# Optimization experiments

Measured on AMD Instinct MI355X. Metric: run time of the kernel, lower is better.

Reference implementation:

```python
import jax, jax.numpy as jnp
import numpy as np

SEQ, EMB, QKV = 4096, 1024, 1024

def setup_inputs() -> dict:
    key = jax.random.key(0)
    k_x, k_q, k_k, k_v = jax.random.split(key, 4)
    scale = 1.0 / np.sqrt(EMB)
    return {
        "x": jax.random.normal(k_x, (SEQ, EMB), dtype=jnp.float32),
        "W_q": jax.random.normal(k_q, (EMB, QKV), dtype=jnp.float32) * scale,
        "W_k": jax.random.normal(k_k, (EMB, QKV), dtype=jnp.float32) * scale,
        "W_v": jax.random.normal(k_v, (EMB, QKV), dtype=jnp.float32) * scale,
    }

def reference(x, W_q, W_k, W_v):
    # Single-head scaled dot-product attention, unbatched: x [S, E]
    d_k = W_q.shape[1]
    Q = x @ W_q          # [S, D]
    K = x @ W_k          # [S, D]
    V = x @ W_v          # [S, D]
    scores = (Q @ K.T) * (1.0 / jnp.sqrt(jnp.asarray(d_k, dtype=x.dtype)))  # [S, S]
    attn = jax.nn.softmax(scores, axis=-1)
    return attn @ V      # [S, D]
```

## Files before the change

### kernel.cpp

```cpp
#include <hip/hip_runtime.h>
#include <cstdint>

#define S_DIM 4096
#define E_DIM 1024
#define D_DIM 1024

typedef __bf16 bf16x8 __attribute__((ext_vector_type(8)));
typedef float  f32x4  __attribute__((ext_vector_type(4)));
typedef unsigned short u16x8 __attribute__((ext_vector_type(8)));

__device__ __forceinline__ unsigned short f2bf(float f) {
  unsigned u = __float_as_uint(f);
  unsigned r = (u + 0x7fffu + ((u >> 16) & 1u)) >> 16;
  return (unsigned short)r;
}

__device__ __forceinline__ void lds_copy16(const unsigned short* g, const unsigned short* l) {
  auto gp = reinterpret_cast<__attribute__((address_space(1))) unsigned int*>(
      reinterpret_cast<uintptr_t>(g));
  auto lp = reinterpret_cast<__attribute__((address_space(3))) unsigned int*>(
      reinterpret_cast<uintptr_t>(l));
  __builtin_amdgcn_global_load_lds(gp, lp, 16, 0, 0);
}

__global__ __launch_bounds__(256) void prep_kernel(
    const float* __restrict__ x,
    const float* __restrict__ Wq, const float* __restrict__ Wk, const float* __restrict__ Wv,
    unsigned short* __restrict__ xbf, unsigned short* __restrict__ Wt,
    float* __restrict__ lsum) {
  const int z = blockIdx.z;
  const int tid = threadIdx.x;
  if (z < 3) {
    const float* W = (z == 0) ? Wq : (z == 1 ? Wk : Wv);
    unsigned short* out = Wt + (size_t)z * E_DIM * D_DIM;
    __shared__ unsigned short tile[32][33];
    int bc = blockIdx.x * 32, br = blockIdx.y * 32;
    int tx = tid & 31, ty = tid >> 5;
#pragma unroll
    for (int i = 0; i < 32; i += 8)
      tile[ty + i][tx] = f2bf(W[(size_t)(br + ty + i) * D_DIM + bc + tx]);
    __syncthreads();
#pragma unroll
    for (int i = 0; i < 32; i += 8)
      out[(size_t)(bc + ty + i) * E_DIM + br + tx] = tile[tx][ty + i];
  } else {
    int bid = blockIdx.y * 32 + blockIdx.x;
    int i = (bid * 256 + tid) * 16;
#pragma unroll
    for (int h = 0; h < 2; h++) {
      float4 a = *(const float4*)(x + i + h * 8);
      float4 b = *(const float4*)(x + i + h * 8 + 4);
      u16x8 o;
      o[0] = f2bf(a.x); o[1] = f2bf(a.y); o[2] = f2bf(a.z); o[3] = f2bf(a.w);
      o[4] = f2bf(b.x); o[5] = f2bf(b.y); o[6] = f2bf(b.z); o[7] = f2bf(b.w);
      *(u16x8*)(xbf + i + h * 8) = o;
    }
    if (bid < 16) lsum[bid * 256 + tid] = 0.f;
  }
}

__global__ __launch_bounds__(256) void transpose_bf16_kernel(
    const unsigned short* __restrict__ in, unsigned short* __restrict__ out,
    int ldin, int ldout) {
  __shared__ unsigned short tile[32][33];
  int bc = blockIdx.x * 32, br = blockIdx.y * 32;
  int tx = threadIdx.x & 31, ty = threadIdx.x >> 5;
#pragma unroll
  for (int i = 0; i < 32; i += 8)
    tile[ty + i][tx] = in[(size_t)(br + ty + i) * ldin + bc + tx];
  __syncthreads();
#pragma unroll
  for (int i = 0; i < 32; i += 8)
    out[(size_t)(bc + ty + i) * ldout + br + tx] = tile[tx][ty + i];
}

template <int MODE, bool SPLIT3>
__global__ __launch_bounds__(256, 2) void gemm_bt_kernel(
    const unsigned short* __restrict__ A, int lda,
    const unsigned short* __restrict__ Bt, int ldb,
    void* __restrict__ Cp, unsigned short* __restrict__ C1,
    unsigned short* __restrict__ C2, int ldc,
    int Kper, float scale, float* __restrict__ lsum) {
  __shared__ __align__(16) unsigned short sA[128 * 64];
  __shared__ __align__(16) unsigned short sB[128 * 64];

  const int tid = threadIdx.x;

  int flat = blockIdx.y * gridDim.x + blockIdx.x;
  int numInG = 8 * gridDim.x;
  int g = flat / numInG;
  int r = flat - g * numInG;
  const int bm = (g * 8 + (r & 7)) * 128;
  const int bn = (r >> 3) * 128;

  const int wave = tid >> 6;
  const int lane = tid & 63;
  const int q    = lane >> 4;
  const int l16  = lane & 15;
  const int wm   = (wave >> 1) * 64;
  const int wn   = (wave & 1) * 64;

  f32x4 zero = {0.f, 0.f, 0.f, 0.f};
  f32x4 acc[4][4];
#pragma unroll
  for (int t = 0; t < 4; t++)
#pragma unroll
    for (int u = 0; u < 4; u++) acc[t][u] = zero;

  const int srow   = tid >> 3;
  const int schunk = (tid & 7) ^ (srow & 3);
  const int kbase  = blockIdx.z * Kper;
  const unsigned short* ap = A  + (size_t)(bm + srow) * lda + kbase + schunk * 8;
  const unsigned short* bp = Bt + (size_t)(bn + srow) * ldb + kbase + schunk * 8;
  unsigned short* saw = sA + wave * 512;
  unsigned short* sbw = sB + wave * 512;
  const size_t stepA = (size_t)32 * lda;
  const size_t stepB = (size_t)32 * ldb;

  const int sw = (q ^ (l16 & 3)) * 8;

  for (int k0 = 0; k0 < Kper; k0 += 64) {
#pragma unroll
    for (int p = 0; p < 4; p++) {
      lds_copy16(ap + k0 + p * stepA, saw + p * 2048);
      lds_copy16(bp + k0 + p * stepB, sbw + p * 2048);
    }
    __syncthreads();

#pragma unroll
    for (int h = 0; h < 2; h++) {
      bf16x8 af[4], bfv[4];
#pragma unroll
      for (int t = 0; t < 4; t++)
        af[t] = *reinterpret_cast<const bf16x8*>(sA + (wm + t * 16 + l16) * 64 + h * 32 + sw);
#pragma unroll
      for (int u = 0; u < 4; u++)
        bfv[u] = *reinterpret_cast<const bf16x8*>(sB + (wn + u * 16 + l16) * 64 + h * 32 + sw);
#pragma unroll
      for (int t = 0; t < 4; t++)
#pragma unroll
        for (int u = 0; u < 4; u++)
          acc[t][u] = __builtin_amdgcn_mfma_f32_16x16x32_bf16(af[t], bfv[u], acc[t][u], 0, 0, 0);
    }
    __syncthreads();
  }

  unsigned short* cb16 = (unsigned short*)Cp;
  int coloff = bn;
  if constexpr (SPLIT3) {
    int which = bn >> 10;
    cb16 = (which == 0) ? (unsigned short*)Cp : (which == 1 ? C1 : C2);
    coloff = bn & 1023;
  }

#pragma unroll
  for (int t = 0; t < 4; t++) {
#pragma unroll
    for (int rr = 0; rr < 4; rr++) {
      const int row = bm + wm + t * 16 + q * 4 + rr;
      float invl = 1.0f;
      if constexpr (MODE == 2) invl = 1.0f / lsum[row];
      float rs = 0.f;
#pragma unroll
      for (int u = 0; u < 4; u++) {
        const int col = coloff + wn + u * 16 + l16;
        float v = acc[t][u][rr] * scale;
        if constexpr (MODE == 0) {
          cb16[(size_t)row * ldc + col] = f2bf(v);
        } else if constexpr (MODE == 1) {
          float p = __expf(v - 8.0f);
          rs += p;
          cb16[(size_t)row * ldc + col] = f2bf(p);
        } else {
          unsafeAtomicAdd((float*)Cp + (size_t)row * ldc + col, acc[t][u][rr] * invl);
        }
      }
      if constexpr (MODE == 1) {
        rs += __shfl_xor(rs, 1);
        rs += __shfl_xor(rs, 2);
        rs += __shfl_xor(rs, 4);
        rs += __shfl_xor(rs, 8);
        if (l16 == 0) unsafeAtomicAdd(&lsum[row], rs);
      }
    }
  }
}

extern "C" void kernel_launch(void* const* d_in, const int* in_sizes, int n_in,
                              void* d_out, int out_size, void* d_ws, size_t ws_size,
                              hipStream_t stream) {
  const float* x  = (const float*)d_in[0];
  const float* Wq = (const float*)d_in[1];
  const float* Wk = (const float*)d_in[2];
  const float* Wv = (const float*)d_in[3];
  float* out = (float*)d_out;

  char* ws = (char*)d_ws;
  const size_t MB = 1024 * 1024;
  unsigned short* SP   = (unsigned short*)(ws);
  unsigned short* Vtmp = (unsigned short*)(ws);
  unsigned short* xbf  = (unsigned short*)(ws + 8 * MB);
  unsigned short* Wt   = (unsigned short*)(ws + 16 * MB);
  unsigned short* Qbf  = (unsigned short*)(ws + 32 * MB);
  unsigned short* Kbf  = (unsigned short*)(ws + 40 * MB);
  unsigned short* Vt   = (unsigned short*)(ws + 48 * MB);
  float*          lsum = (float*)(ws + 56 * MB);

  dim3 blk(256);

  dim3 prgrid(32, 32, 4);
  prep_kernel<<<prgrid, blk, 0, stream>>>(x, Wq, Wk, Wv, xbf, Wt, lsum);

  dim3 pgrid(24, 32, 1);
  gemm_bt_kernel<0, true><<<pgrid, blk, 0, stream>>>(
      xbf, E_DIM, Wt, E_DIM, Qbf, Kbf, Vtmp, D_DIM, E_DIM, 1.0f, nullptr);

  dim3 vtgrid(32, 128);
  transpose_bf16_kernel<<<vtgrid, blk, 0, stream>>>(Vtmp, Vt, D_DIM, S_DIM);

  dim3 sgrid(32, 32, 1);
  gemm_bt_kernel<1, false><<<sgrid, blk, 0, stream>>>(
      Qbf, D_DIM, Kbf, D_DIM, SP, nullptr, nullptr, S_DIM, D_DIM, 0.03125f, lsum);

  hipMemsetAsync(out, 0, (size_t)S_DIM * D_DIM * sizeof(float), stream);
  dim3 ogrid(8, 32, 2);
  gemm_bt_kernel<2, false><<<ogrid, blk, 0, stream>>>(
      SP, S_DIM, Vt, S_DIM, out, nullptr, nullptr, D_DIM, S_DIM / 2, 1.0f, lsum);
}
```

Measured before the change: 224.2 us.

## Use 256x256 tiles with double-buffered LDS pipeline and phased MFMA scheduling

Replaces the 128x128 single-buffered GEMM with a 512-thread, 256x256-tile kernel. It double-buffers LDS and issues the global-to-LDS copies for tile t+2 between MFMA phases, using explicit vmcnt waits, barriers and setprio to overlap loads with compute. Larger tiles raise data reuse per LDS load. The output GEMM's split-K grows from 2 to 4. The change risks lower occupancy (128KB LDS per block), fewer blocks for small grids, and more atomic traffic in the final GEMM.

```diff
diff --git a/kernel.cpp b/kernel.cpp
--- a/kernel.cpp
+++ b/kernel.cpp
@@ -74,75 +74,150 @@
     out[(size_t)(bc + ty + i) * ldout + br + tx] = tile[tx][ty + i];
 }
 
+
+#define PHASE(MH, NH)                                                              \
+  do {                                                                             \
+    asm volatile("s_barrier" ::: "memory");                                        \
+    __builtin_amdgcn_sched_barrier(0);                                             \
+    __builtin_amdgcn_s_setprio(1);                                                 \
+    _Pragma("unroll")                                                              \
+    for (int f_ = 0; f_ < 4; ++f_) {                                               \
+      _Pragma("unroll")                                                            \
+      for (int g_ = 0; g_ < 2; ++g_) {                                             \
+        acc[(MH)*4 + f_][(NH)*2 + g_] = __builtin_amdgcn_mfma_f32_16x16x32_bf16(   \
+            Af[(MH)*4 + f_][0], Bf[g_][0], acc[(MH)*4 + f_][(NH)*2 + g_], 0, 0, 0);\
+        acc[(MH)*4 + f_][(NH)*2 + g_] = __builtin_amdgcn_mfma_f32_16x16x32_bf16(   \
+            Af[(MH)*4 + f_][1], Bf[g_][1], acc[(MH)*4 + f_][(NH)*2 + g_], 0, 0, 0);\
+      }                                                                            \
+    }                                                                              \
+    __builtin_amdgcn_sched_barrier(0);                                             \
+    __builtin_amdgcn_s_setprio(0);                                                 \
+    asm volatile("s_barrier" ::: "memory");                                        \
+  } while (0)
+
 template <int MODE, bool SPLIT3>
-__global__ __launch_bounds__(256, 2) void gemm_bt_kernel(
+__global__ __launch_bounds__(512, 2) void gemm256_kernel(
     const unsigned short* __restrict__ A, int lda,
     const unsigned short* __restrict__ Bt, int ldb,
     void* __restrict__ Cp, unsigned short* __restrict__ C1,
     unsigned short* __restrict__ C2, int ldc,
     int Kper, float scale, float* __restrict__ lsum) {
-  __shared__ __align__(16) unsigned short sA[128 * 64];
-  __shared__ __align__(16) unsigned short sB[128 * 64];
-
-  const int tid = threadIdx.x;
+  __shared__ __align__(16) unsigned short sAB[2][2][16384];
+
+  const int tid  = threadIdx.x;
+  const int wave = tid >> 6;
+  const int lane = tid & 63;
+  const int q    = lane >> 4;
+  const int l16  = lane & 15;
+  const int lx   = l16 & 7;
 
   int flat = blockIdx.y * gridDim.x + blockIdx.x;
   int numInG = 8 * gridDim.x;
   int g = flat / numInG;
   int r = flat - g * numInG;
-  const int bm = (g * 8 + (r & 7)) * 128;
-  const int bn = (r >> 3) * 128;
-
-  const int wave = tid >> 6;
-  const int lane = tid & 63;
-  const int q    = lane >> 4;
-  const int l16  = lane & 15;
-  const int wm   = (wave >> 1) * 64;
-  const int wn   = (wave & 1) * 64;
-
+  const int bm = (g * 8 + (r & 7)) * 256;
+  const int bn = (r >> 3) * 256;
+
+  const int wm = (wave >> 2) * 128;
+  const int wn = (wave & 3) * 64;
+
+  const int kbase = blockIdx.z * Kper;
+  const int NT    = Kper >> 6;
+
+  const int srow = tid >> 3;
+  const int schk = (tid & 7) ^ (srow & 7);
+  const unsigned short* ap = A  + (size_t)(bm + srow) * lda + kbase + schk * 8;
+  const unsigned short* bp = Bt + (size_t)(bn + srow) * ldb + kbase + schk * 8;
+
+  const int aBase = (wm + l16) * 64 + (q ^ lx) * 8;
+  const int bBase = (wn + l16) * 64 + (q ^ lx) * 8;
+
+  f32x4 acc[8][4];
   f32x4 zero = {0.f, 0.f, 0.f, 0.f};
-  f32x4 acc[4][4];
-#pragma unroll
-  for (int t = 0; t < 4; t++)
+#pragma unroll
+  for (int t = 0; t < 8; t++)
 #pragma unroll
     for (int u = 0; u < 4; u++) acc[t][u] = zero;
 
-  const int srow   = tid >> 3;
-  const int schunk = (tid & 7) ^ (srow & 3);
-  const int kbase  = blockIdx.z * Kper;
-  const unsigned short* ap = A  + (size_t)(bm + srow) * lda + kbase + schunk * 8;
-  const unsigned short* bp = Bt + (size_t)(bn + srow) * ldb + kbase + schunk * 8;
-  unsigned short* saw = sA + wave * 512;
-  unsigned short* sbw = sB + wave * 512;
-  const size_t stepA = (size_t)32 * lda;
-  const size_t stepB = (size_t)32 * ldb;
-
-  const int sw = (q ^ (l16 & 3)) * 8;
-
-  for (int k0 = 0; k0 < Kper; k0 += 64) {
-#pragma unroll
-    for (int p = 0; p < 4; p++) {
-      lds_copy16(ap + k0 + p * stepA, saw + p * 2048);
-      lds_copy16(bp + k0 + p * stepB, sbw + p * 2048);
-    }
-    __syncthreads();
-
-#pragma unroll
-    for (int h = 0; h < 2; h++) {
-      bf16x8 af[4], bfv[4];
-#pragma unroll
-      for (int t = 0; t < 4; t++)
-        af[t] = *reinterpret_cast<const bf16x8*>(sA + (wm + t * 16 + l16) * 64 + h * 32 + sw);
-#pragma unroll
-      for (int u = 0; u < 4; u++)
-        bfv[u] = *reinterpret_cast<const bf16x8*>(sB + (wn + u * 16 + l16) * 64 + h * 32 + sw);
-#pragma unroll
-      for (int t = 0; t < 4; t++)
-#pragma unroll
-        for (int u = 0; u < 4; u++)
-          acc[t][u] = __builtin_amdgcn_mfma_f32_16x16x32_bf16(af[t], bfv[u], acc[t][u], 0, 0, 0);
-    }
-    __syncthreads();
+#pragma unroll
+  for (int p = 0; p < 4; ++p)
+    lds_copy16(ap + (size_t)p * 64 * lda, &sAB[0][0][p * 4096 + wave * 512]);
+#pragma unroll
+  for (int p = 0; p < 4; ++p)
+    lds_copy16(bp + (size_t)p * 64 * ldb, &sAB[0][1][p * 4096 + wave * 512]);
+  if (NT > 1) {
+#pragma unroll
+    for (int p = 0; p < 4; ++p)
+      lds_copy16(ap + 64 + (size_t)p * 64 * lda, &sAB[1][0][p * 4096 + wave * 512]);
+#pragma unroll
+    for (int p = 0; p < 4; ++p)
+      lds_copy16(bp + 64 + (size_t)p * 64 * ldb, &sAB[1][1][p * 4096 + wave * 512]);
+    asm volatile("s_waitcnt vmcnt(8)" ::: "memory");
+  } else {
+    asm volatile("s_waitcnt vmcnt(0)" ::: "memory");
+  }
+  asm volatile("s_barrier" ::: "memory");
+
+  for (int t = 0; t < NT; ++t) {
+    const int b = t & 1;
+    const unsigned short* la = &sAB[b][0][0];
+    const unsigned short* lb = &sAB[b][1][0];
+    const bool doSt = (t + 2 < NT);
+    const unsigned short* as_ = ap + (t + 2) * 64;
+    const unsigned short* bs_ = bp + (t + 2) * 64;
+    unsigned short* da = &sAB[b][0][wave * 512];
+    unsigned short* db = &sAB[b][1][wave * 512];
+
+    bf16x8 Af[8][2], Bf[2][2];
+
+#pragma unroll
+    for (int f = 0; f < 4; ++f) {
+      Af[f][0] = *(const bf16x8*)(la + aBase + f * 1024);
+      Af[f][1] = *(const bf16x8*)(la + (aBase ^ 32) + f * 1024);
+    }
+#pragma unroll
+    for (int gg = 0; gg < 2; ++gg) {
+      Bf[gg][0] = *(const bf16x8*)(lb + bBase + gg * 1024);
+      Bf[gg][1] = *(const bf16x8*)(lb + (bBase ^ 32) + gg * 1024);
+    }
+    PHASE(0, 0);
+
+#pragma unroll
+    for (int f = 4; f < 8; ++f) {
+      Af[f][0] = *(const bf16x8*)(la + aBase + f * 1024);
+      Af[f][1] = *(const bf16x8*)(la + (aBase ^ 32) + f * 1024);
+    }
+    PHASE(1, 0);
+
+#pragma unroll
+    for (int gg = 0; gg < 2; ++gg) {
+      Bf[gg][0] = *(const bf16x8*)(lb + bBase + (2 + gg) * 1024);
+      Bf[gg][1] = *(const bf16x8*)(lb + (bBase ^ 32) + (2 + gg) * 1024);
+    }
+    if (doSt) {
+      lds_copy16(as_, da);
+      lds_copy16(as_ + (size_t)64 * lda, da + 4096);
+    }
+    PHASE(0, 1);
+
+    if (doSt) {
+      lds_copy16(as_ + (size_t)128 * lda, da + 8192);
+      lds_copy16(as_ + (size_t)192 * lda, da + 12288);
+      lds_copy16(bs_, db);
+      lds_copy16(bs_ + (size_t)64 * ldb, db + 4096);
+    }
+    PHASE(1, 1);
+
+    if (t + 1 < NT) {
+      if (doSt) {
+        lds_copy16(bs_ + (size_t)128 * ldb, db + 8192);
+        lds_copy16(bs_ + (size_t)192 * ldb, db + 12288);
+        asm volatile("s_waitcnt vmcnt(8)" ::: "memory");
+      } else {
+        asm volatile("s_waitcnt vmcnt(0)" ::: "memory");
+      }
+      asm volatile("s_barrier" ::: "memory");
+    }
   }
 
   unsigned short* cb16 = (unsigned short*)Cp;
@@ -154,17 +229,17 @@
   }
 
 #pragma unroll
-  for (int t = 0; t < 4; t++) {
-#pragma unroll
-    for (int rr = 0; rr < 4; rr++) {
-      const int row = bm + wm + t * 16 + q * 4 + rr;
+  for (int fm = 0; fm < 8; ++fm) {
+#pragma unroll
+    for (int rr = 0; rr < 4; ++rr) {
+      const int row = bm + wm + fm * 16 + q * 4 + rr;
       float invl = 1.0f;
       if constexpr (MODE == 2) invl = 1.0f / lsum[row];
       float rs = 0.f;
 #pragma unroll
-      for (int u = 0; u < 4; u++) {
-        const int col = coloff + wn + u * 16 + l16;
-        float v = acc[t][u][rr] * scale;
+      for (int fn = 0; fn < 4; ++fn) {
+        const int col = coloff + wn + fn * 16 + l16;
+        float v = acc[fm][fn][rr] * scale;
         if constexpr (MODE == 0) {
           cb16[(size_t)row * ldc + col] = f2bf(v);
         } else if constexpr (MODE == 1) {
@@ -172,7 +247,7 @@
           rs += p;
           cb16[(size_t)row * ldc + col] = f2bf(p);
         } else {
-          unsafeAtomicAdd((float*)Cp + (size_t)row * ldc + col, acc[t][u][rr] * invl);
+          unsafeAtomicAdd((float*)Cp + (size_t)row * ldc + col, acc[fm][fn][rr] * invl);
         }
       }
       if constexpr (MODE == 1) {
@@ -206,24 +281,24 @@
   unsigned short* Vt   = (unsigned short*)(ws + 48 * MB);
   float*          lsum = (float*)(ws + 56 * MB);
 
-  dim3 blk(256);
+  dim3 blk(256), blk512(512);
 
   dim3 prgrid(32, 32, 4);
   prep_kernel<<<prgrid, blk, 0, stream>>>(x, Wq, Wk, Wv, xbf, Wt, lsum);
 
-  dim3 pgrid(24, 32, 1);
-  gemm_bt_kernel<0, true><<<pgrid, blk, 0, stream>>>(
+  dim3 pgrid(12, 16, 1);
+  gemm256_kernel<0, true><<<pgrid, blk512, 0, stream>>>(
       xbf, E_DIM, Wt, E_DIM, Qbf, Kbf, Vtmp, D_DIM, E_DIM, 1.0f, nullptr);
 
   dim3 vtgrid(32, 128);
   transpose_bf16_kernel<<<vtgrid, blk, 0, stream>>>(Vtmp, Vt, D_DIM, S_DIM);
 
-  dim3 sgrid(32, 32, 1);
-  gemm_bt_kernel<1, false><<<sgrid, blk, 0, stream>>>(
+  dim3 sgrid(16, 16, 1);
+  gemm256_kernel<1, false><<<sgrid, blk512, 0, stream>>>(
       Qbf, D_DIM, Kbf, D_DIM, SP, nullptr, nullptr, S_DIM, D_DIM, 0.03125f, lsum);
 
   hipMemsetAsync(out, 0, (size_t)S_DIM * D_DIM * sizeof(float), stream);
-  dim3 ogrid(8, 32, 2);
-  gemm_bt_kernel<2, false><<<ogrid, blk, 0, stream>>>(
-      SP, S_DIM, Vt, S_DIM, out, nullptr, nullptr, D_DIM, S_DIM / 2, 1.0f, lsum);
-}
+  dim3 ogrid(4, 16, 4);
+  gemm256_kernel<2, false><<<ogrid, blk512, 0, stream>>>(
+      SP, S_DIM, Vt, S_DIM, out, nullptr, nullptr, D_DIM, S_DIM / 4, 1.0f, lsum);
+}
```

New measurement: 250.9 us. 11.9% more time.

## Widen LDS XOR swizzle to 8 chunks and replace split-K atomics with reduce kernel

Applied to the files above, without the earlier changes.

The shared-memory tile swizzle now XORs the 16-byte chunk index with the low three row bits instead of two, across all eight chunks of a 64-element row. The fragment reads use the matching pattern, which is meant to cut LDS bank conflicts in all three GEMMs. The output GEMM no longer zeroes the output and atomically adds scaled results. Each split-K half instead writes plain fp32 partials, one into a workspace buffer and one into the output, and a new elementwise kernel sums them and applies the softmax 1/l normalization. This removes the memset and the atomics, at the cost of an extra launch and an extra read/write pass over the output.

```diff
diff --git a/kernel.cpp b/kernel.cpp
--- a/kernel.cpp
+++ b/kernel.cpp
@@ -75,7 +75,7 @@
 }
 
 template <int MODE, bool SPLIT3>
-__global__ __launch_bounds__(256, 2) void gemm_bt_kernel(
+__device__ __forceinline__ void gemm_body(
     const unsigned short* __restrict__ A, int lda,
     const unsigned short* __restrict__ Bt, int ldb,
     void* __restrict__ Cp, unsigned short* __restrict__ C1,
@@ -97,6 +97,7 @@
   const int lane = tid & 63;
   const int q    = lane >> 4;
   const int l16  = lane & 15;
+  const int lx   = l16 & 7;
   const int wm   = (wave >> 1) * 64;
   const int wn   = (wave & 1) * 64;
 
@@ -108,7 +109,7 @@
     for (int u = 0; u < 4; u++) acc[t][u] = zero;
 
   const int srow   = tid >> 3;
-  const int schunk = (tid & 7) ^ (srow & 3);
+  const int schunk = (tid & 7) ^ (srow & 7);
   const int kbase  = blockIdx.z * Kper;
   const unsigned short* ap = A  + (size_t)(bm + srow) * lda + kbase + schunk * 8;
   const unsigned short* bp = Bt + (size_t)(bn + srow) * ldb + kbase + schunk * 8;
@@ -117,8 +118,6 @@
   const size_t stepA = (size_t)32 * lda;
   const size_t stepB = (size_t)32 * ldb;
 
-  const int sw = (q ^ (l16 & 3)) * 8;
-
   for (int k0 = 0; k0 < Kper; k0 += 64) {
 #pragma unroll
     for (int p = 0; p < 4; p++) {
@@ -130,12 +129,13 @@
 #pragma unroll
     for (int h = 0; h < 2; h++) {
       bf16x8 af[4], bfv[4];
+      const int pc = (((h << 2) | q) ^ lx) * 8;
 #pragma unroll
       for (int t = 0; t < 4; t++)
-        af[t] = *reinterpret_cast<const bf16x8*>(sA + (wm + t * 16 + l16) * 64 + h * 32 + sw);
+        af[t] = *reinterpret_cast<const bf16x8*>(sA + (wm + t * 16 + l16) * 64 + pc);
 #pragma unroll
       for (int u = 0; u < 4; u++)
-        bfv[u] = *reinterpret_cast<const bf16x8*>(sB + (wn + u * 16 + l16) * 64 + h * 32 + sw);
+        bfv[u] = *reinterpret_cast<const bf16x8*>(sB + (wn + u * 16 + l16) * 64 + pc);
 #pragma unroll
       for (int t = 0; t < 4; t++)
 #pragma unroll
@@ -146,20 +146,21 @@
   }
 
   unsigned short* cb16 = (unsigned short*)Cp;
+  float* o32 = nullptr;
   int coloff = bn;
   if constexpr (SPLIT3) {
     int which = bn >> 10;
     cb16 = (which == 0) ? (unsigned short*)Cp : (which == 1 ? C1 : C2);
     coloff = bn & 1023;
   }
+  if constexpr (MODE == 2)
+    o32 = (blockIdx.z == 0) ? (float*)Cp : (float*)C1;
 
 #pragma unroll
   for (int t = 0; t < 4; t++) {
 #pragma unroll
     for (int rr = 0; rr < 4; rr++) {
       const int row = bm + wm + t * 16 + q * 4 + rr;
-      float invl = 1.0f;
-      if constexpr (MODE == 2) invl = 1.0f / lsum[row];
       float rs = 0.f;
 #pragma unroll
       for (int u = 0; u < 4; u++) {
@@ -172,7 +173,7 @@
           rs += p;
           cb16[(size_t)row * ldc + col] = f2bf(p);
         } else {
-          unsafeAtomicAdd((float*)Cp + (size_t)row * ldc + col, acc[t][u][rr] * invl);
+          o32[(size_t)row * ldc + col] = v;
         }
       }
       if constexpr (MODE == 1) {
@@ -186,6 +187,49 @@
   }
 }
 
+__global__ __launch_bounds__(256, 2) void qkv_gemm(
+    const unsigned short* __restrict__ A, int lda,
+    const unsigned short* __restrict__ Bt, int ldb,
+    void* __restrict__ Cp, unsigned short* __restrict__ C1,
+    unsigned short* __restrict__ C2, int ldc, int Kper, float scale,
+    float* __restrict__ lsum) {
+  gemm_body<0, true>(A, lda, Bt, ldb, Cp, C1, C2, ldc, Kper, scale, lsum);
+}
+__global__ __launch_bounds__(256, 2) void s_gemm(
+    const unsigned short* __restrict__ A, int lda,
+    const unsigned short* __restrict__ Bt, int ldb,
+    void* __restrict__ Cp, unsigned short* __restrict__ C1,
+    unsigned short* __restrict__ C2, int ldc, int Kper, float scale,
+    float* __restrict__ lsum) {
+  gemm_body<1, false>(A, lda, Bt, ldb, Cp, C1, C2, ldc, Kper, scale, lsum);
+}
+__global__ __launch_bounds__(256, 2) void o_gemm(
+    const unsigned short* __restrict__ A, int lda,
+    const unsigned short* __restrict__ Bt, int ldb,
+    void* __restrict__ Cp, unsigned short* __restrict__ C1,
+    unsigned short* __restrict__ C2, int ldc, int Kper, float scale,
+    float* __restrict__ lsum) {
+  gemm_body<2, false>(A, lda, Bt, ldb, Cp, C1, C2, ldc, Kper, scale, lsum);
+}
+
+__global__ __launch_bounds__(256) void reduce_out_kernel(
+    float* __restrict__ out, const float* __restrict__ part,
+    const float* __restrict__ lsum) {
+  const int n4 = (S_DIM * D_DIM) >> 2;
+  const int stride = gridDim.x * blockDim.x;
+  for (int v = blockIdx.x * blockDim.x + threadIdx.x; v < n4; v += stride) {
+    float inv = 1.0f / lsum[v >> 8];
+    float4 a = reinterpret_cast<const float4*>(out)[v];
+    float4 b = reinterpret_cast<const float4*>(part)[v];
+    float4 o;
+    o.x = (a.x + b.x) * inv;
+    o.y = (a.y + b.y) * inv;
+    o.z = (a.z + b.z) * inv;
+    o.w = (a.w + b.w) * inv;
+    reinterpret_cast<float4*>(out)[v] = o;
+  }
+}
+
 extern "C" void kernel_launch(void* const* d_in, const int* in_sizes, int n_in,
                               void* d_out, int out_size, void* d_ws, size_t ws_size,
                               hipStream_t stream) {
@@ -204,6 +248,7 @@
   unsigned short* Qbf  = (unsigned short*)(ws + 32 * MB);
   unsigned short* Kbf  = (unsigned short*)(ws + 40 * MB);
   unsigned short* Vt   = (unsigned short*)(ws + 48 * MB);
+  float*          Prt  = (float*)(ws + 32 * MB);
   float*          lsum = (float*)(ws + 56 * MB);
 
   dim3 blk(256);
@@ -212,18 +257,20 @@
   prep_kernel<<<prgrid, blk, 0, stream>>>(x, Wq, Wk, Wv, xbf, Wt, lsum);
 
   dim3 pgrid(24, 32, 1);
-  gemm_bt_kernel<0, true><<<pgrid, blk, 0, stream>>>(
+  qkv_gemm<<<pgrid, blk, 0, stream>>>(
       xbf, E_DIM, Wt, E_DIM, Qbf, Kbf, Vtmp, D_DIM, E_DIM, 1.0f, nullptr);
 
   dim3 vtgrid(32, 128);
   transpose_bf16_kernel<<<vtgrid, blk, 0, stream>>>(Vtmp, Vt, D_DIM, S_DIM);
 
   dim3 sgrid(32, 32, 1);
-  gemm_bt_kernel<1, false><<<sgrid, blk, 0, stream>>>(
+  s_gemm<<<sgrid, blk, 0, stream>>>(
       Qbf, D_DIM, Kbf, D_DIM, SP, nullptr, nullptr, S_DIM, D_DIM, 0.03125f, lsum);
 
-  hipMemsetAsync(out, 0, (size_t)S_DIM * D_DIM * sizeof(float), stream);
   dim3 ogrid(8, 32, 2);
-  gemm_bt_kernel<2, false><<<ogrid, blk, 0, stream>>>(
-      SP, S_DIM, Vt, S_DIM, out, nullptr, nullptr, D_DIM, S_DIM / 2, 1.0f, lsum);
-}
+  o_gemm<<<ogrid, blk, 0, stream>>>(
+      SP, S_DIM, Vt, S_DIM, Prt, (unsigned short*)out, nullptr, D_DIM, S_DIM / 2,
+      1.0f, nullptr);
+
+  reduce_out_kernel<<<dim3(2048), blk, 0, stream>>>(out, Prt, lsum);
+}
```

New measurement: 208.4 us. -7.0%, faster.

## Compute V transposed directly, drop split-K atomics, widen LDS swizzle

Applied to the files above, without the earlier changes.

V^T is now produced directly as a GEMM of W_v^T against x, which removes the separate transpose kernel and its extra memory pass. The output GEMM no longer splits K in two with atomic adds; it uses a 64-wide N tile with plain stores, so the memset is also gone. The LDS XOR swizzle is widened from 2 to 3 bits to cut bank conflicts. In exchange, the output GEMM's tiles each do less MFMA work per load, which may lower its arithmetic intensity.

```diff
diff --git a/kernel.cpp b/kernel.cpp
--- a/kernel.cpp
+++ b/kernel.cpp
@@ -59,30 +59,15 @@
   }
 }
 
-__global__ __launch_bounds__(256) void transpose_bf16_kernel(
-    const unsigned short* __restrict__ in, unsigned short* __restrict__ out,
-    int ldin, int ldout) {
-  __shared__ unsigned short tile[32][33];
-  int bc = blockIdx.x * 32, br = blockIdx.y * 32;
-  int tx = threadIdx.x & 31, ty = threadIdx.x >> 5;
-#pragma unroll
-  for (int i = 0; i < 32; i += 8)
-    tile[ty + i][tx] = in[(size_t)(br + ty + i) * ldin + bc + tx];
-  __syncthreads();
-#pragma unroll
-  for (int i = 0; i < 32; i += 8)
-    out[(size_t)(bc + ty + i) * ldout + br + tx] = tile[tx][ty + i];
-}
-
-template <int MODE, bool SPLIT3>
-__global__ __launch_bounds__(256, 2) void gemm_bt_kernel(
-    const unsigned short* __restrict__ A, int lda,
-    const unsigned short* __restrict__ Bt, int ldb,
-    void* __restrict__ Cp, unsigned short* __restrict__ C1,
-    unsigned short* __restrict__ C2, int ldc,
-    int Kper, float scale, float* __restrict__ lsum) {
+template <int MODE, int NSPLIT, int BN>
+__device__ __forceinline__ void gemm_body(
+    const unsigned short* __restrict__ A, int lda,
+    const unsigned short* __restrict__ Bt, int ldb,
+    void* __restrict__ Cp, unsigned short* __restrict__ C1, int ldc,
+    int Kper, float scale, float* __restrict__ lsum) {
+  constexpr int NF = BN / 32;
   __shared__ __align__(16) unsigned short sA[128 * 64];
-  __shared__ __align__(16) unsigned short sB[128 * 64];
+  __shared__ __align__(16) unsigned short sB[BN * 64];
 
   const int tid = threadIdx.x;
 
@@ -91,55 +76,55 @@
   int g = flat / numInG;
   int r = flat - g * numInG;
   const int bm = (g * 8 + (r & 7)) * 128;
-  const int bn = (r >> 3) * 128;
+  const int bn = (r >> 3) * BN;
 
   const int wave = tid >> 6;
   const int lane = tid & 63;
   const int q    = lane >> 4;
   const int l16  = lane & 15;
+  const int lx   = l16 & 7;
   const int wm   = (wave >> 1) * 64;
-  const int wn   = (wave & 1) * 64;
+  const int wn   = (wave & 1) * (BN / 2);
 
   f32x4 zero = {0.f, 0.f, 0.f, 0.f};
-  f32x4 acc[4][4];
+  f32x4 acc[4][NF];
 #pragma unroll
   for (int t = 0; t < 4; t++)
 #pragma unroll
-    for (int u = 0; u < 4; u++) acc[t][u] = zero;
+    for (int u = 0; u < NF; u++) acc[t][u] = zero;
 
   const int srow   = tid >> 3;
-  const int schunk = (tid & 7) ^ (srow & 3);
-  const int kbase  = blockIdx.z * Kper;
-  const unsigned short* ap = A  + (size_t)(bm + srow) * lda + kbase + schunk * 8;
-  const unsigned short* bp = Bt + (size_t)(bn + srow) * ldb + kbase + schunk * 8;
+  const int schunk = (tid & 7) ^ (srow & 7);
+  const unsigned short* ap = A  + (size_t)(bm + srow) * lda + schunk * 8;
+  const unsigned short* bp = Bt + (size_t)(bn + srow) * ldb + schunk * 8;
   unsigned short* saw = sA + wave * 512;
   unsigned short* sbw = sB + wave * 512;
   const size_t stepA = (size_t)32 * lda;
   const size_t stepB = (size_t)32 * ldb;
 
-  const int sw = (q ^ (l16 & 3)) * 8;
-
   for (int k0 = 0; k0 < Kper; k0 += 64) {
 #pragma unroll
-    for (int p = 0; p < 4; p++) {
+    for (int p = 0; p < 4; p++)
       lds_copy16(ap + k0 + p * stepA, saw + p * 2048);
+#pragma unroll
+    for (int p = 0; p < NF; p++)
       lds_copy16(bp + k0 + p * stepB, sbw + p * 2048);
-    }
     __syncthreads();
 
 #pragma unroll
     for (int h = 0; h < 2; h++) {
-      bf16x8 af[4], bfv[4];
+      bf16x8 af[4], bfv[NF];
+      const int pc = (((h << 2) | q) ^ lx) * 8;
 #pragma unroll
       for (int t = 0; t < 4; t++)
-        af[t] = *reinterpret_cast<const bf16x8*>(sA + (wm + t * 16 + l16) * 64 + h * 32 + sw);
-#pragma unroll
-      for (int u = 0; u < 4; u++)
-        bfv[u] = *reinterpret_cast<const bf16x8*>(sB + (wn + u * 16 + l16) * 64 + h * 32 + sw);
+        af[t] = *reinterpret_cast<const bf16x8*>(sA + (wm + t * 16 + l16) * 64 + pc);
+#pragma unroll
+      for (int u = 0; u < NF; u++)
+        bfv[u] = *reinterpret_cast<const bf16x8*>(sB + (wn + u * 16 + l16) * 64 + pc);
 #pragma unroll
       for (int t = 0; t < 4; t++)
 #pragma unroll
-        for (int u = 0; u < 4; u++)
+        for (int u = 0; u < NF; u++)
           acc[t][u] = __builtin_amdgcn_mfma_f32_16x16x32_bf16(af[t], bfv[u], acc[t][u], 0, 0, 0);
     }
     __syncthreads();
@@ -147,11 +132,11 @@
 
   unsigned short* cb16 = (unsigned short*)Cp;
   int coloff = bn;
-  if constexpr (SPLIT3) {
-    int which = bn >> 10;
-    cb16 = (which == 0) ? (unsigned short*)Cp : (which == 1 ? C1 : C2);
+  if constexpr (NSPLIT == 2) {
+    if (bn >= 1024) cb16 = C1;
     coloff = bn & 1023;
   }
+  float* o32 = (float*)Cp;
 
 #pragma unroll
   for (int t = 0; t < 4; t++) {
@@ -162,7 +147,7 @@
       if constexpr (MODE == 2) invl = 1.0f / lsum[row];
       float rs = 0.f;
 #pragma unroll
-      for (int u = 0; u < 4; u++) {
+      for (int u = 0; u < NF; u++) {
         const int col = coloff + wn + u * 16 + l16;
         float v = acc[t][u][rr] * scale;
         if constexpr (MODE == 0) {
@@ -172,7 +157,7 @@
           rs += p;
           cb16[(size_t)row * ldc + col] = f2bf(p);
         } else {
-          unsafeAtomicAdd((float*)Cp + (size_t)row * ldc + col, acc[t][u][rr] * invl);
+          o32[(size_t)row * ldc + col] = acc[t][u][rr] * invl;
         }
       }
       if constexpr (MODE == 1) {
@@ -186,6 +171,35 @@
   }
 }
 
+__global__ __launch_bounds__(256, 2) void qk_gemm(
+    const unsigned short* __restrict__ A, int lda,
+    const unsigned short* __restrict__ Bt, int ldb,
+    void* __restrict__ Cp, unsigned short* __restrict__ C1, int ldc,
+    int Kper, float scale, float* __restrict__ lsum) {
+  gemm_body<0, 2, 128>(A, lda, Bt, ldb, Cp, C1, ldc, Kper, scale, lsum);
+}
+__global__ __launch_bounds__(256, 2) void vt_gemm(
+    const unsigned short* __restrict__ A, int lda,
+    const unsigned short* __restrict__ Bt, int ldb,
+    void* __restrict__ Cp, unsigned short* __restrict__ C1, int ldc,
+    int Kper, float scale, float* __restrict__ lsum) {
+  gemm_body<0, 1, 128>(A, lda, Bt, ldb, Cp, C1, ldc, Kper, scale, lsum);
+}
+__global__ __launch_bounds__(256, 2) void s_gemm(
+    const unsigned short* __restrict__ A, int lda,
+    const unsigned short* __restrict__ Bt, int ldb,
+    void* __restrict__ Cp, unsigned short* __restrict__ C1, int ldc,
+    int Kper, float scale, float* __restrict__ lsum) {
+  gemm_body<1, 1, 128>(A, lda, Bt, ldb, Cp, C1, ldc, Kper, scale, lsum);
+}
+__global__ __launch_bounds__(256, 2) void o_gemm(
+    const unsigned short* __restrict__ A, int lda,
+    const unsigned short* __restrict__ Bt, int ldb,
+    void* __restrict__ Cp, unsigned short* __restrict__ C1, int ldc,
+    int Kper, float scale, float* __restrict__ lsum) {
+  gemm_body<2, 1, 64>(A, lda, Bt, ldb, Cp, C1, ldc, Kper, scale, lsum);
+}
+
 extern "C" void kernel_launch(void* const* d_in, const int* in_sizes, int n_in,
                               void* d_out, int out_size, void* d_ws, size_t ws_size,
                               hipStream_t stream) {
@@ -198,7 +212,6 @@
   char* ws = (char*)d_ws;
   const size_t MB = 1024 * 1024;
   unsigned short* SP   = (unsigned short*)(ws);
-  unsigned short* Vtmp = (unsigned short*)(ws);
   unsigned short* xbf  = (unsigned short*)(ws + 8 * MB);
   unsigned short* Wt   = (unsigned short*)(ws + 16 * MB);
   unsigned short* Qbf  = (unsigned short*)(ws + 32 * MB);
@@ -211,19 +224,20 @@
   dim3 prgrid(32, 32, 4);
   prep_kernel<<<prgrid, blk, 0, stream>>>(x, Wq, Wk, Wv, xbf, Wt, lsum);
 
-  dim3 pgrid(24, 32, 1);
-  gemm_bt_kernel<0, true><<<pgrid, blk, 0, stream>>>(
-      xbf, E_DIM, Wt, E_DIM, Qbf, Kbf, Vtmp, D_DIM, E_DIM, 1.0f, nullptr);
-
-  dim3 vtgrid(32, 128);
-  transpose_bf16_kernel<<<vtgrid, blk, 0, stream>>>(Vtmp, Vt, D_DIM, S_DIM);
-
-  dim3 sgrid(32, 32, 1);
-  gemm_bt_kernel<1, false><<<sgrid, blk, 0, stream>>>(
-      Qbf, D_DIM, Kbf, D_DIM, SP, nullptr, nullptr, S_DIM, D_DIM, 0.03125f, lsum);
-
-  hipMemsetAsync(out, 0, (size_t)S_DIM * D_DIM * sizeof(float), stream);
-  dim3 ogrid(8, 32, 2);
-  gemm_bt_kernel<2, false><<<ogrid, blk, 0, stream>>>(
-      SP, S_DIM, Vt, S_DIM, out, nullptr, nullptr, D_DIM, S_DIM / 2, 1.0f, lsum);
-}
+  dim3 qgrid(16, 32);
+  qk_gemm<<<qgrid, blk, 0, stream>>>(
+      xbf, E_DIM, Wt, E_DIM, Qbf, Kbf, D_DIM, E_DIM, 1.0f, nullptr);
+
+  dim3 vgrid(32, 8);
+  vt_gemm<<<vgrid, blk, 0, stream>>>(
+      Wt + 2 * E_DIM * D_DIM, E_DIM, xbf, E_DIM, Vt, nullptr, S_DIM,
+      E_DIM, 1.0f, nullptr);
+
+  dim3 sgrid(32, 32);
+  s_gemm<<<sgrid, blk, 0, stream>>>(
+      Qbf, D_DIM, Kbf, D_DIM, SP, nullptr, S_DIM, D_DIM, 0.03125f, lsum);
+
+  dim3 ogrid(16, 32);
+  o_gemm<<<ogrid, blk, 0, stream>>>(
+      SP, S_DIM, Vt, S_DIM, out, nullptr, D_DIM, S_DIM, 1.0f, lsum);
+}
```

Measured after the change: 225.0 us. No clear change (+0.4%).
